# Optimization experiments

Measured on AMD Instinct MI355X. Metric: run time of the kernel, lower is better.

## Reference

```python
import jax, jax.numpy as jnp
import numpy as np

DELTA = 16
KAPPA = 4
ACTION_LOSS_WEIGHT = 0.2
ACTION_CLASS_WEIGHT = 10.0
NEG = -1e30  # sentinel for masked-out positions

B, T = 1024, 4096


def setup_inputs() -> dict:
    key = jax.random.key(0)
    k1, k2, k3, k4 = jax.random.split(key, 4)
    s1s2_log_probs = jax.random.normal(k1, (B, T, 2), dtype=jnp.float32)
    action_log_probs = jax.random.normal(k2, (B, T, 1), dtype=jnp.float32)
    lens = jax.random.randint(k3, (B,), T // 2, T + 1, dtype=jnp.int32)
    video_level_scores = jax.random.uniform(k4, (B,), dtype=jnp.float32)
    return {
        "s1s2_log_probs": s1s2_log_probs,
        "action_log_probs": action_log_probs,
        "lens": lens,
        "video_level_scores": video_level_scores,
    }


def _optimal_state_change(s1s2_probs, action_probs, lens):
    """Per-video optimal (state1, action, state2) alignment with delta spacing.

    Maximizes p1[s1] * pa[ac] * p2[s2] s.t. s1 <= ac - DELTA, ac + DELTA <= s2 < len,
    via prefix/suffix cumulative maxima (O(T) DP per video, fully vectorized).
    Returns integer targets: state_targets in {0,1,2}, action_targets in {0,1,2}.
    """
    Bn, Tn, _ = s1s2_probs.shape
    p1, p2 = s1s2_probs[..., 0], s1s2_probs[..., 1]
    pa = action_probs[..., 0]
    t = jnp.arange(Tn)
    valid = t[None, :] < lens[:, None]  # [B,T]
    p1m = jnp.where(valid, p1, NEG)
    p2m = jnp.where(valid, p2, NEG)
    pre = jax.lax.cummax(p1m, axis=1)                                  # max p1[0..t]
    suf = jnp.flip(jax.lax.cummax(jnp.flip(p2m, 1), axis=1), 1)        # max p2[t..T-1]
    pad = jnp.full((Bn, DELTA), NEG, dtype=p1.dtype)
    pre_s = jnp.concatenate([pad, pre[:, : Tn - DELTA]], axis=1)       # best s1 <= ac-DELTA
    suf_s = jnp.concatenate([suf[:, DELTA:], pad], axis=1)             # best s2 >= ac+DELTA
    ok = (pre_s > NEG / 2) & (suf_s > NEG / 2) & valid
    score = jnp.where(ok, pre_s * pa * suf_s, NEG)
    ac = jnp.argmax(score, axis=1)                                     # [B]
    s1 = jnp.argmax(jnp.where(t[None, :] <= (ac - DELTA)[:, None], p1m, NEG), axis=1)
    s2 = jnp.argmax(jnp.where(t[None, :] >= (ac + DELTA)[:, None], p2m, NEG), axis=1)
    state_t = ((t[None, :] == s1[:, None]).astype(jnp.int32)
               + 2 * (t[None, :] == s2[:, None]).astype(jnp.int32))
    dist = jnp.abs(t[None, :] - ac[:, None])
    action_t = jnp.where(valid, jnp.where(dist <= KAPPA, 2, 1), 0)
    return state_t, action_t


def reference(s1s2_log_probs, action_log_probs, lens, video_level_scores):
    s1s2_probs = jax.nn.softmax(s1s2_log_probs, axis=-1)
    action_probs = jax.nn.sigmoid(action_log_probs)
    state_t, action_t = _optimal_state_change(
        jax.lax.stop_gradient(s1s2_probs), jax.lax.stop_gradient(action_probs), lens)

    # state loss: CE over 2 classes, masked where target == 0 (ignore)
    logp = jax.nn.log_softmax(s1s2_log_probs, axis=-1)          # [B,T,2]
    cls = jnp.clip(state_t - 1, 0, None)
    state_loss = -jnp.take_along_axis(logp, cls[..., None], axis=-1)[..., 0]
    state_loss = state_loss * (state_t != 0).astype(logp.dtype)

    # action loss: weighted BCE-with-logits
    z = action_log_probs[..., 0]                                 # [B,T]
    y = (action_t == 2).astype(z.dtype)
    bce = jnp.maximum(z, 0.0) - z * y + jnp.log1p(jnp.exp(-jnp.abs(z)))
    w = (action_t == 1).astype(z.dtype) + ACTION_CLASS_WEIGHT * (action_t == 2).astype(z.dtype)
    action_loss = bce * w

    state_loss = state_loss * video_level_scores[:, None]
    action_loss = action_loss * video_level_scores[:, None]
    return jnp.sum(state_loss), ACTION_LOSS_WEIGHT * jnp.sum(action_loss)
```

## Files before the change

kernel.cpp:

```cpp
#include <hip/hip_runtime.h>
#include <math.h>


#define T_LEN 4096
#define NCH   256
#define CH    16
#define PADS  17
#define NEGV  (-1e30f)
#define NEGH  (-5e29f)

__device__ __forceinline__ float frcp(float x) { return __builtin_amdgcn_rcpf(x); }

__device__ __forceinline__ void amax_comb(float& v, int& i, float ov, int oi) {
  if (ov > v || (ov == v && oi < i)) { v = ov; i = oi; }
}

__global__ __launch_bounds__(256, 4) void lftc_main(
    const float* __restrict__ s1s2,
    const float* __restrict__ act,
    const int*   __restrict__ lens,
    const float* __restrict__ vls,
    float* __restrict__ ws)
{
  __shared__ float P1s[NCH * PADS];
  __shared__ float cm1[NCH];
  __shared__ float cm2[NCH];
  __shared__ float wag1[4], wag2[4];
  __shared__ float redv[4];  __shared__ int redi[4];
  __shared__ float redv2[4]; __shared__ int redi2[4];
  __shared__ float redv3[4]; __shared__ int redi3[4];
  __shared__ int   s_ac;

  const int b    = blockIdx.x;
  const int tid  = threadIdx.x;
  const int lane = tid & 63;
  const int wv   = tid >> 6;
  const int len  = lens[b];
  const float w  = vls[b];

  const float* __restrict__ srow = s1s2 + (size_t)b * T_LEN * 2;
  const float* __restrict__ zrow = act  + (size_t)b * T_LEN;

  const int j    = tid;
  const int base = j * CH;

  float4 sv[8];
  {
    const float4* sp4 = reinterpret_cast<const float4*>(srow + 2 * base);
#pragma unroll
    for (int k = 0; k < 8; k++) sv[k] = sp4[k];
  }
  float4 zv[4];
  {
    const float4* zp4 = reinterpret_cast<const float4*>(zrow + base);
#pragma unroll
    for (int k = 0; k < 4; k++) zv[k] = zp4[k];
  }
  const float* sf = reinterpret_cast<const float*>(sv);
  float z[16];
  {
    const float* zf = reinterpret_cast<const float*>(zv);
#pragma unroll
    for (int i = 0; i < 16; i++) z[i] = zf[i];
  }

  float m1 = NEGV, m2 = NEGV, sp_part = 0.f;
#pragma unroll
  for (int i = 0; i < CH; i++) {
    float lx = sf[2 * i], ly = sf[2 * i + 1];
    float p  = frcp(1.f + __expf(ly - lx));
    bool  v  = (base + i) < len;
    float p1m = v ? p : NEGV;
    float p2m = v ? 1.f - p : NEGV;
    P1s[j * PADS + i] = p1m;
    m1 = fmaxf(m1, p1m);
    m2 = fmaxf(m2, p2m);
    float zi = z[i];
    if (v) sp_part += fmaxf(zi, 0.f) + __logf(1.f + __expf(-fabsf(zi)));
  }

  {
    float pm = m1;
#pragma unroll
    for (int off = 1; off < 64; off <<= 1) {
      float o = __shfl_up(pm, off);
      if (lane >= off) pm = fmaxf(pm, o);
    }
    float sm = m2;
#pragma unroll
    for (int off = 1; off < 64; off <<= 1) {
      float o = __shfl_down(sm, off);
      if (lane + off < 64) sm = fmaxf(sm, o);
    }
    if (lane == 63) wag1[wv] = pm;
    if (lane == 0)  wag2[wv] = sm;
    __syncthreads();
    float addp = NEGV, adds = NEGV;
#pragma unroll
    for (int q = 0; q < 4; q++) {
      if (q < wv) addp = fmaxf(addp, wag1[q]);
      if (q > wv) adds = fmaxf(adds, wag2[q]);
    }
    cm1[tid] = fmaxf(pm, addp);
    cm2[tid] = fmaxf(sm, adds);
    __syncthreads();
  }

  float best = NEGV;
  int   bidx = base;
  {
    float rs[CH];
    if (j <= NCH - 2) {
      float run = (j + 2 <= NCH - 1) ? cm2[j + 2] : NEGV;
      const int b2 = (j + 1) * PADS;
#pragma unroll
      for (int i = CH - 1; i >= 0; --i) {
        float p1n = P1s[b2 + i];
        float p2n = (p1n > NEGH) ? 1.f - p1n : NEGV;
        run = fmaxf(run, p2n);
        rs[i] = run;
      }
    }
    float prerun = (j >= 2) ? cm1[j - 2] : NEGV;
    const int b1 = (j - 1) * PADS;
#pragma unroll
    for (int i = 0; i < CH; i++) {
      float pre_s = NEGV;
      if (j >= 1) { prerun = fmaxf(prerun, P1s[b1 + i]); pre_s = prerun; }
      float suf_s = (j <= NCH - 2) ? rs[i] : NEGV;
      int t = base + i;
      if (pre_s > NEGH && suf_s > NEGH && t < len) {
        float pa = frcp(1.f + __expf(-z[i]));
        float sc = (pre_s * pa) * suf_s;
        if (sc > best) { best = sc; bidx = t; }
      }
    }
  }
#pragma unroll
  for (int off = 32; off; off >>= 1) {
    float ov = __shfl_down(best, off);
    int   oi = __shfl_down(bidx, off);
    amax_comb(best, bidx, ov, oi);
  }
  if (lane == 0) { redv[wv] = best; redi[wv] = bidx; }
  __syncthreads();
  if (tid == 0) {
    float v = redv[0]; int i = redi[0];
    for (int q = 1; q < 4; q++) amax_comb(v, i, redv[q], redi[q]);
    s_ac = i;
  }
  __syncthreads();
  const int ac = s_ac;

  float v1 = NEGV; int i1 = 0;
  float v2 = NEGV; int i2 = 0;
  {
    const int e1   = ac - CH;
    const int s2lo = ac + CH;
#pragma unroll
    for (int k = 0; k < CH; k++) {
      int t = base + k;
      float p1v = P1s[j * PADS + k];
      if (t <= e1 && p1v > v1) { v1 = p1v; i1 = t; }
      float p2v = (p1v > NEGH) ? 1.f - p1v : NEGV;
      if (t >= s2lo && p2v > v2) { v2 = p2v; i2 = t; }
    }
#pragma unroll
    for (int off = 32; off; off >>= 1) {
      float ov1 = __shfl_down(v1, off); int oi1 = __shfl_down(i1, off);
      amax_comb(v1, i1, ov1, oi1);
      float ov2 = __shfl_down(v2, off); int oi2 = __shfl_down(i2, off);
      amax_comb(v2, i2, ov2, oi2);
    }
    if (lane == 0) { redv2[wv] = v1; redi2[wv] = i1; redv3[wv] = v2; redi3[wv] = i2; }
  }

  if (tid < 9) {
    int t = ac - 4 + tid;
    if (t >= 0 && t < len) {
      float zc = zrow[t];
      float b0 = fmaxf(zc, 0.f) + __logf(1.f + __expf(-fabsf(zc)));
      sp_part += 10.f * (b0 - zc) - b0;
    }
  }
  float s = sp_part;
#pragma unroll
  for (int off = 32; off; off >>= 1) s += __shfl_down(s, off);
  if (lane == 0) wag1[wv] = s;
  __syncthreads();
  if (tid == 0) {
    float tot = wag1[0] + wag1[1] + wag1[2] + wag1[3];

    float sv1 = redv2[0]; int s1 = redi2[0];
    float sv2 = redv3[0]; int s2 = redi3[0];
    for (int q = 1; q < 4; q++) {
      amax_comb(sv1, s1, redv2[q], redi2[q]);
      amax_comb(sv2, s2, redv3[q], redi3[q]);
    }
    float a0 = srow[2 * (size_t)s1],     a1 = srow[2 * (size_t)s1 + 1];
    float c0 = srow[2 * (size_t)s2],     c1 = srow[2 * (size_t)s2 + 1];
    float d1 = a1 - a0;
    float loss1 = fmaxf(d1, 0.f) + __logf(1.f + __expf(-fabsf(d1)));
    float d2 = c0 - c1;
    float loss2 = fmaxf(d2, 0.f) + __logf(1.f + __expf(-fabsf(d2)));

    ws[2 * (size_t)b]     = w * (loss1 + loss2);
    ws[2 * (size_t)b + 1] = 0.2f * w * tot;
  }
}

__global__ void lftc_reduce(const float* __restrict__ ws, float* __restrict__ out, int B) {
  __shared__ float a0[4], a1[4];
  const int tid  = threadIdx.x;
  const int lane = tid & 63;
  const int wv   = tid >> 6;
  float s0 = 0.f, s1 = 0.f;
  for (int i = tid; i < B; i += 256) {
    s0 += ws[2 * (size_t)i];
    s1 += ws[2 * (size_t)i + 1];
  }
#pragma unroll
  for (int off = 32; off; off >>= 1) {
    s0 += __shfl_down(s0, off);
    s1 += __shfl_down(s1, off);
  }
  if (lane == 0) { a0[wv] = s0; a1[wv] = s1; }
  __syncthreads();
  if (tid == 0) {
    out[0] = a0[0] + a0[1] + a0[2] + a0[3];
    out[1] = a1[0] + a1[1] + a1[2] + a1[3];
  }
}

extern "C" void kernel_launch(void* const* d_in, const int* in_sizes, int n_in,
                              void* d_out, int out_size, void* d_ws, size_t ws_size,
                              hipStream_t stream) {
  const float* s1s2 = (const float*)d_in[0];
  const float* act  = (const float*)d_in[1];
  const int*   lens = (const int*)d_in[2];
  const float* vls  = (const float*)d_in[3];
  float* out = (float*)d_out;
  float* ws  = (float*)d_ws;

  const int B = in_sizes[2];

  lftc_main<<<B, 256, 0, stream>>>(s1s2, act, lens, vls, ws);
  lftc_reduce<<<1, 256, 0, stream>>>(ws, out, B);
}
```

Baseline: 98.82 us.

## Fuse final reduction into main kernel via last-block atomic counter

Removes the separate single-block reduce kernel. Each block bumps a global atomic counter, and the last block to finish sums the per-video partials and writes the output. It also has every thread redo the small argmax combine itself, which saves one block-wide barrier. In exchange it adds a memset launch for the counter, a threadfence and an atomic in every block. If the timer counts launches, the memset may cancel out the saved launch.

```diff
diff --git a/kernel.cpp b/kernel.cpp
--- a/kernel.cpp
+++ b/kernel.cpp
@@ -8,6 +8,7 @@
 #define PADS  17
 #define NEGV  (-1e30f)
 #define NEGH  (-5e29f)
+#define CTR_F 4096
 
 __device__ __forceinline__ float frcp(float x) { return __builtin_amdgcn_rcpf(x); }
 
@@ -20,7 +21,9 @@
     const float* __restrict__ act,
     const int*   __restrict__ lens,
     const float* __restrict__ vls,
-    float* __restrict__ ws)
+    float* __restrict__ ws,
+    float* __restrict__ out,
+    int B)
 {
   __shared__ float P1s[NCH * PADS];
   __shared__ float cm1[NCH];
@@ -29,7 +32,8 @@
   __shared__ float redv[4];  __shared__ int redi[4];
   __shared__ float redv2[4]; __shared__ int redi2[4];
   __shared__ float redv3[4]; __shared__ int redi3[4];
-  __shared__ int   s_ac;
+  __shared__ float fa0[4], fa1[4];
+  __shared__ int   s_last;
 
   const int b    = blockIdx.x;
   const int tid  = threadIdx.x;
@@ -144,13 +148,13 @@
   }
   if (lane == 0) { redv[wv] = best; redi[wv] = bidx; }
   __syncthreads();
-  if (tid == 0) {
+  int ac;
+  {
     float v = redv[0]; int i = redi[0];
+#pragma unroll
     for (int q = 1; q < 4; q++) amax_comb(v, i, redv[q], redi[q]);
-    s_ac = i;
-  }
-  __syncthreads();
-  const int ac = s_ac;
+    ac = i;
+  }
 
   float v1 = NEGV; int i1 = 0;
   float v2 = NEGV; int i2 = 0;
@@ -191,14 +195,14 @@
   if (tid == 0) {
     float tot = wag1[0] + wag1[1] + wag1[2] + wag1[3];
 
-    float sv1 = redv2[0]; int s1 = redi2[0];
-    float sv2 = redv3[0]; int s2 = redi3[0];
+    float sv1 = redv2[0]; int s1i = redi2[0];
+    float sv2 = redv3[0]; int s2i = redi3[0];
     for (int q = 1; q < 4; q++) {
-      amax_comb(sv1, s1, redv2[q], redi2[q]);
-      amax_comb(sv2, s2, redv3[q], redi3[q]);
-    }
-    float a0 = srow[2 * (size_t)s1],     a1 = srow[2 * (size_t)s1 + 1];
-    float c0 = srow[2 * (size_t)s2],     c1 = srow[2 * (size_t)s2 + 1];
+      amax_comb(sv1, s1i, redv2[q], redi2[q]);
+      amax_comb(sv2, s2i, redv3[q], redi3[q]);
+    }
+    float a0 = srow[2 * (size_t)s1i],     a1 = srow[2 * (size_t)s1i + 1];
+    float c0 = srow[2 * (size_t)s2i],     c1 = srow[2 * (size_t)s2i + 1];
     float d1 = a1 - a0;
     float loss1 = fmaxf(d1, 0.f) + __logf(1.f + __expf(-fabsf(d1)));
     float d2 = c0 - c1;
@@ -206,29 +210,30 @@
 
     ws[2 * (size_t)b]     = w * (loss1 + loss2);
     ws[2 * (size_t)b + 1] = 0.2f * w * tot;
-  }
-}
-
-__global__ void lftc_reduce(const float* __restrict__ ws, float* __restrict__ out, int B) {
-  __shared__ float a0[4], a1[4];
-  const int tid  = threadIdx.x;
-  const int lane = tid & 63;
-  const int wv   = tid >> 6;
-  float s0 = 0.f, s1 = 0.f;
-  for (int i = tid; i < B; i += 256) {
-    s0 += ws[2 * (size_t)i];
-    s1 += ws[2 * (size_t)i + 1];
-  }
-#pragma unroll
-  for (int off = 32; off; off >>= 1) {
-    s0 += __shfl_down(s0, off);
-    s1 += __shfl_down(s1, off);
-  }
-  if (lane == 0) { a0[wv] = s0; a1[wv] = s1; }
+
+    __threadfence();
+    unsigned old = atomicAdd(reinterpret_cast<unsigned int*>(ws + CTR_F), 1u);
+    s_last = (old == (unsigned)(B - 1)) ? 1 : 0;
+  }
   __syncthreads();
-  if (tid == 0) {
-    out[0] = a0[0] + a0[1] + a0[2] + a0[3];
-    out[1] = a1[0] + a1[1] + a1[2] + a1[3];
+
+  if (s_last) {
+    float s0 = 0.f, s1 = 0.f;
+    for (int i = tid; i < B; i += 256) {
+      s0 += __hip_atomic_load(ws + 2 * (size_t)i,     __ATOMIC_RELAXED, __HIP_MEMORY_SCOPE_AGENT);
+      s1 += __hip_atomic_load(ws + 2 * (size_t)i + 1, __ATOMIC_RELAXED, __HIP_MEMORY_SCOPE_AGENT);
+    }
+#pragma unroll
+    for (int off = 32; off; off >>= 1) {
+      s0 += __shfl_down(s0, off);
+      s1 += __shfl_down(s1, off);
+    }
+    if (lane == 0) { fa0[wv] = s0; fa1[wv] = s1; }
+    __syncthreads();
+    if (tid == 0) {
+      out[0] = fa0[0] + fa0[1] + fa0[2] + fa0[3];
+      out[1] = fa1[0] + fa1[1] + fa1[2] + fa1[3];
+    }
   }
 }
 
@@ -244,6 +249,6 @@
 
   const int B = in_sizes[2];
 
-  lftc_main<<<B, 256, 0, stream>>>(s1s2, act, lens, vls, ws);
-  lftc_reduce<<<1, 256, 0, stream>>>(ws, out, B);
+  hipMemsetAsync((char*)d_ws + CTR_F * sizeof(float), 0, sizeof(unsigned int), stream);
+  lftc_main<<<B, 256, 0, stream>>>(s1s2, act, lens, vls, ws, out, B);
 }
```

Result: slower. 110.0 us (+11.3%).
